# Kernel optimization log

Hardware: AMD Instinct MI355X
Metric: run time of the kernel (lower is better)

## Reference

```python
import jax, jax.numpy as jnp
import numpy as np

D = 64; H = 8; HD = 8; L = 3; FFN = 256
MAX_CHUNKS = 1024; MCL = 16


def rms_norm(x, w, eps=1e-6):
    return x * w * jax.lax.rsqrt(jnp.mean(x * x, axis=-1, keepdims=True) + eps)


def rope(x):
    # x: [B, S, H, HD]
    S, hd = x.shape[1], x.shape[-1]
    half = hd // 2
    freqs = 1.0 / (10000.0 ** (jnp.arange(half, dtype=x.dtype) * 2.0 / hd))
    ang = jnp.arange(S, dtype=x.dtype)[:, None] * freqs  # [S, half]
    cos = jnp.cos(ang)[None, :, None, :]
    sin = jnp.sin(ang)[None, :, None, :]
    x1, x2 = x[..., :half], x[..., half:]
    return jnp.concatenate([x1 * cos - x2 * sin, x1 * sin + x2 * cos], axis=-1)


def block(x, wq, wk, wv, wo, g1, g2, w1, w2):
    B, S, _ = x.shape
    h = rms_norm(x, g1)
    q = rope((h @ wq).reshape(B, S, H, HD))
    k = rope((h @ wk).reshape(B, S, H, HD))
    v = (h @ wv).reshape(B, S, H, HD)
    scores = jnp.einsum('bqhd,bkhd->bhqk', q, k) / jnp.sqrt(jnp.asarray(HD, x.dtype))
    causal = jnp.tril(jnp.ones((S, S), dtype=bool))
    scores = jnp.where(causal, scores, jnp.asarray(-1e30, x.dtype))
    attn = jax.nn.softmax(scores, axis=-1)
    o = jnp.einsum('bhqk,bkhd->bqhd', attn, v).reshape(B, S, D)
    x = x + o @ wo
    h2 = rms_norm(x, g2)
    return x + jax.nn.gelu(h2 @ w1, approximate=False) @ w2


def setup_inputs() -> dict:
    key = jax.random.key(0)
    ks = jax.random.split(key, 12)
    B, S = 4, 2048
    s = 1.0 / np.sqrt(D)
    return {
        'x': jax.random.normal(ks[0], (B, S, D), jnp.float32),
        'pad_token_vector': jax.random.normal(ks[1], (D,), jnp.float32),
        'x_ids': jax.random.randint(ks[2], (B, S), 0, 256),
        'pad_token_id': 257,
        'Wq': jax.random.normal(ks[3], (L, D, D), jnp.float32) * s,
        'Wk': jax.random.normal(ks[4], (L, D, D), jnp.float32) * s,
        'Wv': jax.random.normal(ks[5], (L, D, D), jnp.float32) * s,
        'Wo': jax.random.normal(ks[6], (L, D, D), jnp.float32) * s,
        'ln1': jnp.ones((L, D), jnp.float32),
        'ln2': jnp.ones((L, D), jnp.float32),
        'W1': jax.random.normal(ks[7], (L, D, FFN), jnp.float32) * s,
        'W2': jax.random.normal(ks[8], (L, FFN, D), jnp.float32) * (1.0 / np.sqrt(FFN)),
        'Whead': jax.random.normal(ks[9], (D, 2), jnp.float32) * s,
        'bhead': jnp.zeros((2,), jnp.float32),
    }


def reference(x, pad_token_vector, x_ids, pad_token_id, Wq, Wk, Wv, Wo, ln1, ln2, W1, W2, Whead, bhead):
    B, S, _ = x.shape
    h = x
    for l in range(L):
        h = block(h, Wq[l], Wk[l], Wv[l], Wo[l], ln1[l], ln2[l], W1[l], W2[l])
    logits = h @ Whead + bhead  # [B, S, 2]
    end_mask = logits[..., 0] > logits[..., 1]  # [B, S]
    t = jnp.arange(S)
    # fallback: if a row has no end, mark the last position as an end
    has_end = jnp.any(end_mask, axis=-1, keepdims=True)
    end_mask = jnp.where(has_end, end_mask, t[None, :] == S - 1)
    em = end_mask.astype(jnp.int32)
    num_ends = jnp.sum(em, axis=-1)                 # [B] = number of chunks
    chunk_id = jnp.cumsum(em, axis=-1) - em         # exclusive count of prior ends
    prev_end = jnp.concatenate([jnp.ones((B, 1), bool), end_mask[:, :-1]], axis=1)
    start_marker = jnp.where(prev_end, t[None, :], -1)
    start = jax.lax.associative_scan(jnp.maximum, start_marker, axis=-1)  # cummax -> chunk start per token
    pos = t[None, :] - start                        # position within chunk
    valid = (chunk_id < num_ends[:, None]) & (chunk_id < MAX_CHUNKS) & (pos < MCL)
    c_idx = jnp.where(valid, chunk_id, MAX_CHUNKS)  # invalid -> dummy chunk, sliced off
    p_idx = jnp.where(valid, pos, 0)
    b_idx = jnp.arange(B)[:, None]
    out = jnp.broadcast_to(pad_token_vector, (B, MAX_CHUNKS + 1, MCL, D))
    out = out.at[b_idx, c_idx, p_idx].set(h)[:, :MAX_CHUNKS]
    ids = jnp.full((B, MAX_CHUNKS + 1, MCL), pad_token_id, dtype=x_ids.dtype)
    ids = ids.at[b_idx, c_idx, p_idx].set(x_ids)[:, :MAX_CHUNKS]
    reg_term = jnp.mean(logits[..., 1])
    return out, ids, reg_term
```

## Files before the change

kernel.cpp:

```cpp
#include <hip/hip_runtime.h>
#include <math.h>

constexpr int D   = 64;
constexpr int H   = 8;
constexpr int HD  = 8;
constexpr int NL  = 3;
constexpr int FFNx= 256;
constexpr int Bb  = 4;
constexpr int Ss  = 2048;
constexpr int NT  = Bb * Ss;
constexpr int MAXC= 1024;
constexpr int MCL = 16;

constexpr int TPB  = 72;
constexpr int BPB  = 36;
constexpr int PBSZ = 2304;

constexpr size_t WX  = 0;
constexpr size_t WQ  = 524288;
constexpr size_t WKV = 2621440;
constexpr size_t WPB = 4194304;
constexpr size_t WL1 = 9764864;
constexpr size_t WEM = WL1 + NT;
constexpr size_t WINV= WEM + NT;
constexpr size_t WCT = WINV + Bb*MAXC*MCL;
constexpr size_t WST = WCT + Ss*4;

constexpr float LOG2E = 1.4426950408889634f;

typedef float v2f  __attribute__((ext_vector_type(2)));
typedef float f16v __attribute__((ext_vector_type(16)));
using ckv_t = const __attribute__((address_space(4))) f16v*;

__device__ __forceinline__ float rdlane(float v, int l) {
    return __builtin_bit_cast(float, __builtin_amdgcn_readlane(__builtin_bit_cast(int, v), l));
}

__global__ void k_init(const float* __restrict__ x, float* __restrict__ X,
                       float* __restrict__ ct, float* __restrict__ st) {
    int i = blockIdx.x * blockDim.x + threadIdx.x;
    constexpr int N4 = NT * D / 4;
    if (i < N4) ((float4*)X)[i] = ((const float4*)x)[i];
    if (i < Ss * 4) {
        int s = i >> 2, f = i & 3;
        const float fr[4] = {1.0f, 0.1f, 0.01f, 0.001f};
        float ang = (float)s * fr[f];
        ct[i] = cosf(ang);
        st[i] = sinf(ang);
    }
}

__global__ __launch_bounds__(256) void k_qkv(
    const float* __restrict__ X, const float* __restrict__ Wq,
    const float* __restrict__ Wk, const float* __restrict__ Wv,
    const float* __restrict__ g1, const float* __restrict__ ct,
    const float* __restrict__ st, float* __restrict__ Q,
    float* __restrict__ KV) {
    __shared__ float wq_s[D*D], wk_s[D*D], wv_s[D*D];
    __shared__ float g_s[D];
    int tid = threadIdx.x;
    for (int i = tid; i < D*D; i += 256) {
        wq_s[i] = Wq[i]; wk_s[i] = Wk[i]; wv_s[i] = Wv[i];
    }
    if (tid < D) g_s[tid] = g1[tid];
    __syncthreads();
    int w = tid >> 6, d = tid & 63;
    int t0 = blockIdx.x * 16;
    for (int it = 0; it < 4; ++it) {
        int t = t0 + it*4 + w;
        float xv = X[t*D + d];
        float ss = xv * xv;
        #pragma unroll
        for (int off = 32; off; off >>= 1) ss += __shfl_xor(ss, off);
        float r = 1.0f / sqrtf(ss * (1.0f/D) + 1e-6f);
        float h = xv * g_s[d] * r;
        float aq = 0.f, ak = 0.f, av = 0.f;
        #pragma unroll
        for (int j = 0; j < D; ++j) {
            float hj = rdlane(h, j);
            aq += hj * wq_s[j*D + d];
            ak += hj * wk_s[j*D + d];
            av += hj * wv_s[j*D + d];
        }
        int s  = t & (Ss - 1);
        int e  = d & 7;
        int fi = e & 3;
        float c  = ct[s*4 + fi];
        float sn = st[s*4 + fi];
        float pq = __shfl_xor(aq, 4);
        float pk = __shfl_xor(ak, 4);
        float rq, rk;
        if (e < 4) { rq = aq*c - pq*sn; rk = ak*c - pk*sn; }
        else       { rq = pq*sn + aq*c; rk = pk*sn + ak*c; }
        Q[t*D + d] = rq;
        int bq = t >> 11;
        int hh = d >> 3;
        float* kvp = KV + ((((size_t)(bq*H + hh))*Ss + s) << 4);
        kvp[e]     = rk;
        kvp[8 + e] = av;
    }
}

template<int DIAG>
__device__ __forceinline__ void attn_loop4(
    ckv_t kvs, int L, int rel0,
    const v2f* __restrict__ qp0, const v2f* __restrict__ qp1,
    v2f& l0, v2f& l1, v2f* __restrict__ o0, v2f* __restrict__ o1) {
    #pragma unroll 4
    for (int j = 0; j < 64; ++j) {
        f16v kv = kvs[j];
        v2f a1;
        a1  = qp1[0] * (v2f){kv[0], kv[0]};
        a1 += qp1[1] * (v2f){kv[1], kv[1]};
        a1 += qp1[2] * (v2f){kv[2], kv[2]};
        a1 += qp1[3] * (v2f){kv[3], kv[3]};
        a1 += qp1[4] * (v2f){kv[4], kv[4]};
        a1 += qp1[5] * (v2f){kv[5], kv[5]};
        a1 += qp1[6] * (v2f){kv[6], kv[6]};
        a1 += qp1[7] * (v2f){kv[7], kv[7]};
        if (DIAG == 2) {
            int rel = rel0 + j;
            if (rel > L)      a1.x = -1e30f;
            if (rel > L + 64) a1.y = -1e30f;
        }
        v2f p1;
        p1.x = __builtin_amdgcn_exp2f(a1.x);
        p1.y = __builtin_amdgcn_exp2f(a1.y);
        l1 += p1;
        o1[0] += p1 * (v2f){kv[8],  kv[8]};
        o1[1] += p1 * (v2f){kv[9],  kv[9]};
        o1[2] += p1 * (v2f){kv[10], kv[10]};
        o1[3] += p1 * (v2f){kv[11], kv[11]};
        o1[4] += p1 * (v2f){kv[12], kv[12]};
        o1[5] += p1 * (v2f){kv[13], kv[13]};
        o1[6] += p1 * (v2f){kv[14], kv[14]};
        o1[7] += p1 * (v2f){kv[15], kv[15]};
        if (DIAG != 2) {
            v2f a0;
            a0  = qp0[0] * (v2f){kv[0], kv[0]};
            a0 += qp0[1] * (v2f){kv[1], kv[1]};
            a0 += qp0[2] * (v2f){kv[2], kv[2]};
            a0 += qp0[3] * (v2f){kv[3], kv[3]};
            a0 += qp0[4] * (v2f){kv[4], kv[4]};
            a0 += qp0[5] * (v2f){kv[5], kv[5]};
            a0 += qp0[6] * (v2f){kv[6], kv[6]};
            a0 += qp0[7] * (v2f){kv[7], kv[7]};
            if (DIAG == 1) {
                int rel = rel0 + j;
                if (rel > L)      a0.x = -1e30f;
                if (rel > L + 64) a0.y = -1e30f;
            }
            v2f p0;
            p0.x = __builtin_amdgcn_exp2f(a0.x);
            p0.y = __builtin_amdgcn_exp2f(a0.y);
            l0 += p0;
            o0[0] += p0 * (v2f){kv[8],  kv[8]};
            o0[1] += p0 * (v2f){kv[9],  kv[9]};
            o0[2] += p0 * (v2f){kv[10], kv[10]};
            o0[3] += p0 * (v2f){kv[11], kv[11]};
            o0[4] += p0 * (v2f){kv[12], kv[12]};
            o0[5] += p0 * (v2f){kv[13], kv[13]};
            o0[6] += p0 * (v2f){kv[14], kv[14]};
            o0[7] += p0 * (v2f){kv[15], kv[15]};
        }
    }
}

__global__ __launch_bounds__(256) void k_attn2(
    const float* __restrict__ Qg, const float* __restrict__ KV,
    float* __restrict__ PB) {
    __shared__ float comb[2][PBSZ];
    int xcd  = blockIdx.x & 7;
    int slot = blockIdx.x >> 3;
    int bhg  = slot / BPB;
    int blk  = slot - bhg * BPB;
    int bh   = bhg * 8 + xcd;
    int wvu  = __builtin_amdgcn_readfirstlane(threadIdx.x >> 6);
    int pair = wvu >> 1;
    int half = wvu & 1;
    int widb = blk * 2 + pair;
    int L = threadIdx.x & 63;
    int rem = widb;
    int s = 0;
    while (rem >= 8 - (s >> 1)) { rem -= 8 - (s >> 1); ++s; }
    int t = (s >> 1) + rem;
    int b = bh >> 3, h = bh & 7;
    int qmin = t * 256;
    int k0 = s * 128 + half * 64;

    const float SC = 0.35355339059327373f * LOG2E;
    const float* qp = Qg + ((size_t)(b*Ss + qmin + L))*D + h*HD;
    float4 qa0 = *(const float4*)(qp);
    float4 qb0 = *(const float4*)(qp + 4);
    float4 qa1 = *(const float4*)(qp + 64*D);
    float4 qb1 = *(const float4*)(qp + 64*D + 4);
    float4 qa2 = *(const float4*)(qp + 128*D);
    float4 qb2 = *(const float4*)(qp + 128*D + 4);
    float4 qa3 = *(const float4*)(qp + 192*D);
    float4 qb3 = *(const float4*)(qp + 192*D + 4);
    v2f qp0[8], qp1[8];
    qp0[0] = (v2f){qa0.x*SC, qa1.x*SC};  qp1[0] = (v2f){qa2.x*SC, qa3.x*SC};
    qp0[1] = (v2f){qa0.y*SC, qa1.y*SC};  qp1[1] = (v2f){qa2.y*SC, qa3.y*SC};
    qp0[2] = (v2f){qa0.z*SC, qa1.z*SC};  qp1[2] = (v2f){qa2.z*SC, qa3.z*SC};
    qp0[3] = (v2f){qa0.w*SC, qa1.w*SC};  qp1[3] = (v2f){qa2.w*SC, qa3.w*SC};
    qp0[4] = (v2f){qb0.x*SC, qb1.x*SC};  qp1[4] = (v2f){qb2.x*SC, qb3.x*SC};
    qp0[5] = (v2f){qb0.y*SC, qb1.y*SC};  qp1[5] = (v2f){qb2.y*SC, qb3.y*SC};
    qp0[6] = (v2f){qb0.z*SC, qb1.z*SC};  qp1[6] = (v2f){qb2.z*SC, qb3.z*SC};
    qp0[7] = (v2f){qb0.w*SC, qb1.w*SC};  qp1[7] = (v2f){qb2.w*SC, qb3.w*SC};

    v2f l0 = (v2f){0.f, 0.f}, l1 = (v2f){0.f, 0.f};
    v2f o0[8], o1[8];
    #pragma unroll
    for (int e = 0; e < 8; ++e) { o0[e] = (v2f){0.f, 0.f}; o1[e] = (v2f){0.f, 0.f}; }

    ckv_t kvs = (ckv_t)(unsigned long long)(KV + (((size_t)bh*Ss + k0) << 4));
    if (s == 2*t)          attn_loop4<1>(kvs, L, half*64, qp0, qp1, l0, l1, o0, o1);
    else if (s == 2*t + 1) attn_loop4<2>(kvs, L, half*64, qp0, qp1, l0, l1, o0, o1);
    else                   attn_loop4<0>(kvs, L, half*64, qp0, qp1, l0, l1, o0, o1);

    if (half == 1) {
        comb[pair][L]       = l0.x;
        comb[pair][64 + L]  = l0.y;
        comb[pair][128 + L] = l1.x;
        comb[pair][192 + L] = l1.y;
        #pragma unroll
        for (int e = 0; e < 8; ++e) {
            comb[pair][256 + e*256 + L]       = o0[e].x;
            comb[pair][256 + e*256 + 64 + L]  = o0[e].y;
            comb[pair][256 + e*256 + 128 + L] = o1[e].x;
            comb[pair][256 + e*256 + 192 + L] = o1[e].y;
        }
    }
    __syncthreads();
    if (half == 0) {
        int pbidx = t*(t+1) + s;
        float* pb = PB + ((size_t)bh * TPB + pbidx) * PBSZ;
        pb[L]       = l0.x + comb[pair][L];
        pb[64 + L]  = l0.y + comb[pair][64 + L];
        pb[128 + L] = l1.x + comb[pair][128 + L];
        pb[192 + L] = l1.y + comb[pair][192 + L];
        #pragma unroll
        for (int e = 0; e < 8; ++e) {
            pb[256 + e*256 + L]       = o0[e].x + comb[pair][256 + e*256 + L];
            pb[256 + e*256 + 64 + L]  = o0[e].y + comb[pair][256 + e*256 + 64 + L];
            pb[256 + e*256 + 128 + L] = o1[e].x + comb[pair][256 + e*256 + 128 + L];
            pb[256 + e*256 + 192 + L] = o1[e].y + comb[pair][256 + e*256 + 192 + L];
        }
    }
}

__global__ __launch_bounds__(256) void k_combo(
    const float* __restrict__ PB, float* __restrict__ X,
    const float* __restrict__ Wo) {
    __shared__ float wo_s[D*D];
    __shared__ float oT[32][65];
    int tid = threadIdx.x;
    int seg = blockIdx.x & 7;
    int t   = (blockIdx.x >> 3) & 7;
    int b   = blockIdx.x >> 6;
    for (int i = tid; i < D*D; i += 256) wo_s[i] = Wo[i];

    int h  = tid >> 5;
    int ql = tid & 31;
    int qs = seg*32 + ql;
    int bh = b*8 + h;
    int nch = 2*(t+1);
    float Lx = 0.f;
    float O[8] = {0,0,0,0,0,0,0,0};
    for (int s3 = 0; s3 < nch; ++s3) {
        int idx = t*(t+1) + s3;
        const float* pb = PB + (size_t)(bh*TPB + idx) * PBSZ;
        Lx += pb[qs];
        #pragma unroll
        for (int e = 0; e < 8; ++e) O[e] += pb[256 + e*256 + qs];
    }
    float inv = 1.0f / Lx;
    #pragma unroll
    for (int e = 0; e < 8; ++e) oT[ql][h*8 + e] = O[e] * inv;
    __syncthreads();

    int d = tid & 63, wv = tid >> 6;
    #pragma unroll 2
    for (int k = 0; k < 8; ++k) {
        int tt = wv*8 + k;
        float a = 0.f;
        #pragma unroll
        for (int j = 0; j < D; ++j) a += oT[tt][j] * wo_s[j*D + d];
        X[((size_t)(b*Ss) + t*256 + seg*32 + tt)*D + d] += a;
    }
}

template<bool HEAD>
__global__ __launch_bounds__(256) void k_ffn(
    float* __restrict__ X, const float* __restrict__ g2,
    const float* __restrict__ W1, const float* __restrict__ W2,
    const float* __restrict__ Wh, const float* __restrict__ bhp,
    float* __restrict__ logit1, int* __restrict__ em) {
    __shared__ __align__(16) float h2t[64][20];
    __shared__ float part[16][16];
    __shared__ float g_s[D];
    __shared__ __align__(16) float ult[FFNx][20];
    __shared__ float red[4][16][D];
    int tid = threadIdx.x;
    if (tid < D) g_s[tid] = g2[tid];
    int t0 = blockIdx.x * 16;
    int tk = tid >> 4, li = tid & 15;
    float x0 = X[(t0+tk)*D + li];
    float x1 = X[(t0+tk)*D + li + 16];
    float x2 = X[(t0+tk)*D + li + 32];
    float x3 = X[(t0+tk)*D + li + 48];
    part[tk][li] = x0*x0 + x1*x1 + x2*x2 + x3*x3;
    __syncthreads();
    if (tid < 16) {
        float s = 0.f;
        #pragma unroll
        for (int i = 0; i < 16; ++i) s += part[tid][i];
        part[tid][0] = 1.0f / sqrtf(s * (1.0f/D) + 1e-6f);
    }
    __syncthreads();
    float r = part[tk][0];
    h2t[li][tk]      = x0 * g_s[li]      * r;
    h2t[li + 16][tk] = x1 * g_s[li + 16] * r;
    h2t[li + 32][tk] = x2 * g_s[li + 32] * r;
    h2t[li + 48][tk] = x3 * g_s[li + 48] * r;
    __syncthreads();
    {
        int f = tid;
        v2f acc2[8];
        #pragma unroll
        for (int i = 0; i < 8; ++i) acc2[i] = (v2f){0.f, 0.f};
        for (int j = 0; j < D; ++j) {
            float wv = W1[j*FFNx + f];
            v2f wv2 = (v2f){wv, wv};
            const float4* hp = (const float4*)&h2t[j][0];
            float4 a0 = hp[0], a1 = hp[1], a2 = hp[2], a3 = hp[3];
            const v2f* a0v = (const v2f*)&a0;
            const v2f* a1v = (const v2f*)&a1;
            const v2f* a2v = (const v2f*)&a2;
            const v2f* a3v = (const v2f*)&a3;
            acc2[0] += a0v[0]*wv2;  acc2[1] += a0v[1]*wv2;
            acc2[2] += a1v[0]*wv2;  acc2[3] += a1v[1]*wv2;
            acc2[4] += a2v[0]*wv2;  acc2[5] += a2v[1]*wv2;
            acc2[6] += a3v[0]*wv2;  acc2[7] += a3v[1]*wv2;
        }
        #pragma unroll
        for (int i = 0; i < 8; ++i) {
            float ua = acc2[i].x;
            float ub = acc2[i].y;
            ua = 0.5f * ua * (1.0f + erff(ua * 0.70710678118654752f));
            ub = 0.5f * ub * (1.0f + erff(ub * 0.70710678118654752f));
            ult[f][2*i]     = ua;
            ult[f][2*i + 1] = ub;
        }
    }
    __syncthreads();
    {
        int d = tid & 63, fp = tid >> 6;
        v2f acc2[8];
        #pragma unroll
        for (int i = 0; i < 8; ++i) acc2[i] = (v2f){0.f, 0.f};
        for (int fo = 0; fo < 64; ++fo) {
            int f = fp*64 + fo;
            float wv = W2[f*D + d];
            v2f wv2 = (v2f){wv, wv};
            const float4* up = (const float4*)&ult[f][0];
            float4 u0 = up[0], u1 = up[1], u2 = up[2], u3 = up[3];
            const v2f* u0v = (const v2f*)&u0;
            const v2f* u1v = (const v2f*)&u1;
            const v2f* u2v = (const v2f*)&u2;
            const v2f* u3v = (const v2f*)&u3;
            acc2[0] += u0v[0]*wv2;  acc2[1] += u0v[1]*wv2;
            acc2[2] += u1v[0]*wv2;  acc2[3] += u1v[1]*wv2;
            acc2[4] += u2v[0]*wv2;  acc2[5] += u2v[1]*wv2;
            acc2[6] += u3v[0]*wv2;  acc2[7] += u3v[1]*wv2;
        }
        #pragma unroll
        for (int i = 0; i < 8; ++i) {
            red[fp][2*i][d]     = acc2[i].x;
            red[fp][2*i + 1][d] = acc2[i].y;
        }
        __syncthreads();
        int tk2 = tid >> 6;
        #pragma unroll
        for (int k = 0; k < 4; ++k) {
            int tt = tk2 + k*4;
            float sum = red[0][tt][d] + red[1][tt][d] + red[2][tt][d] + red[3][tt][d];
            float xf = X[(t0 + tt)*D + d] + sum;
            X[(t0 + tt)*D + d] = xf;
            if (HEAD) {
                float p0 = xf * Wh[d*2];
                float p1 = xf * Wh[d*2 + 1];
                #pragma unroll
                for (int off = 32; off; off >>= 1) {
                    p0 += __shfl_xor(p0, off);
                    p1 += __shfl_xor(p1, off);
                }
                if (d == 0) {
                    float l0 = p0 + bhp[0], l1 = p1 + bhp[1];
                    em[t0 + tt] = (l0 > l1) ? 1 : 0;
                    logit1[t0 + tt] = l1;
                }
            }
        }
    }
}

__global__ void k_reg(const float* __restrict__ logit1, float* __restrict__ outreg) {
    __shared__ float red[256];
    int tid = threadIdx.x;
    float s = 0.f;
    for (int i = tid; i < NT; i += 256) s += logit1[i];
    red[tid] = s;
    __syncthreads();
    for (int off = 128; off; off >>= 1) {
        if (tid < off) red[tid] += red[tid + off];
        __syncthreads();
    }
    if (tid == 0) *outreg = red[0] * (1.0f / NT);
}

__global__ __launch_bounds__(256) void k_scan(const int* __restrict__ em,
                                              int* __restrict__ inv) {
    __shared__ int ssum[256], smax[256];
    __shared__ int sany, stot;
    int b = blockIdx.x, tid = threadIdx.x;
    int* invb = inv + b * (MAXC*MCL);
    for (int i = tid; i < MAXC*MCL; i += 256) invb[i] = -1;
    __syncthreads();
    const int* e = em + b*Ss;
    int base = tid * 8;
    int loc[8];
    int lsum = 0, lor = 0;
    #pragma unroll
    for (int i = 0; i < 8; ++i) { loc[i] = e[base + i]; lsum += loc[i]; lor |= loc[i]; }
    ssum[tid] = lor;
    __syncthreads();
    if (tid == 0) { int a = 0; for (int i = 0; i < 256; ++i) a |= ssum[i]; sany = a; }
    __syncthreads();
    int any = sany;
    __syncthreads();
    if (!any && tid == 255) { loc[7] = 1; lsum = 1; }
    int prev = (tid == 0) ? 1 : e[base - 1];
    if (!any && tid) prev = 0;
    int mk[8];
    int lmax = -1;
    #pragma unroll
    for (int i = 0; i < 8; ++i) {
        int pe = (i == 0) ? prev : loc[i - 1];
        if (i == 7 && !any && tid == 255) pe = e[base + 6];
        mk[i] = pe ? (base + i) : -1;
        lmax = max(lmax, mk[i]);
    }
    ssum[tid] = lsum; smax[tid] = lmax;
    __syncthreads();
    if (tid == 0) {
        int rs = 0, rm = -1;
        for (int i = 0; i < 256; ++i) {
            int ts = ssum[i], tm = smax[i];
            ssum[i] = rs; smax[i] = rm;
            rs += ts; rm = max(rm, tm);
        }
        stot = rs;
    }
    __syncthreads();
    int run = ssum[tid], rmax = smax[tid], tot = stot;
    #pragma unroll
    for (int i = 0; i < 8; ++i) {
        int s = base + i;
        rmax = max(rmax, mk[i]);
        int chunk = run;
        run += loc[i];
        int pos = s - rmax;
        bool valid = (chunk < tot) && (chunk < MAXC) && (pos < MCL);
        if (valid) invb[chunk * MCL + pos] = b*Ss + s;
    }
}

__global__ __launch_bounds__(256) void k_out(
    const float* __restrict__ X, const float* __restrict__ pad,
    const int* __restrict__ xids, const int* __restrict__ padid,
    const int* __restrict__ inv, float* __restrict__ out) {
    int i = blockIdx.x * blockDim.x + threadIdx.x;
    constexpr int NV4 = Bb * MAXC * MCL * D / 4;
    constexpr int NI4 = Bb * MAXC * MCL / 4;
    if (i < NV4) {
        int slot = i >> 4;
        int d4 = i & 15;
        int t = inv[slot];
        float4 v = (t >= 0) ? ((const float4*)X)[t*16 + d4]
                            : ((const float4*)pad)[d4];
        ((float4*)out)[i] = v;
    } else if (i < NV4 + NI4) {
        int j = i - NV4;
        float pv = (float)(*padid);
        int base = j * 4;
        int t0_ = inv[base], t1_ = inv[base+1], t2_ = inv[base+2], t3_ = inv[base+3];
        float4 v;
        v.x = (t0_ >= 0) ? (float)xids[t0_] : pv;
        v.y = (t1_ >= 0) ? (float)xids[t1_] : pv;
        v.z = (t2_ >= 0) ? (float)xids[t2_] : pv;
        v.w = (t3_ >= 0) ? (float)xids[t3_] : pv;
        ((float4*)out)[i] = v;
    }
}

extern "C" void kernel_launch(void* const* d_in, const int* in_sizes, int n_in,
                              void* d_out, int out_size, void* d_ws, size_t ws_size,
                              hipStream_t stream) {
    const float* x    = (const float*)d_in[0];
    const float* pad  = (const float*)d_in[1];
    const int*   xids = (const int*)  d_in[2];
    const int*   padid= (const int*)  d_in[3];
    const float* Wq   = (const float*)d_in[4];
    const float* Wk   = (const float*)d_in[5];
    const float* Wv   = (const float*)d_in[6];
    const float* Wo   = (const float*)d_in[7];
    const float* ln1  = (const float*)d_in[8];
    const float* ln2  = (const float*)d_in[9];
    const float* W1   = (const float*)d_in[10];
    const float* W2   = (const float*)d_in[11];
    const float* Wh   = (const float*)d_in[12];
    const float* bh   = (const float*)d_in[13];
    float* out = (float*)d_out;
    float* ws  = (float*)d_ws;

    float* X  = ws + WX;
    float* Qb = ws + WQ;
    float* KVb= ws + WKV;
    float* PBb= ws + WPB;
    float* L1b= ws + WL1;
    int*   EMb= (int*)(ws + WEM);
    int*   INVb=(int*)(ws + WINV);
    float* ct = ws + WCT;
    float* st = ws + WST;

    k_init<<<2048, 256, 0, stream>>>(x, X, ct, st);
    for (int l = 0; l < NL; ++l) {
        k_qkv <<<512, 256, 0, stream>>>(X, Wq + l*D*D, Wk + l*D*D, Wv + l*D*D,
                                        ln1 + l*D, ct, st, Qb, KVb);
        k_attn2<<<32*BPB, 256, 0, stream>>>(Qb, KVb, PBb);
        k_combo<<<256, 256, 0, stream>>>(PBb, X, Wo + l*D*D);
        if (l == NL - 1)
            k_ffn<true ><<<NT/16, 256, 0, stream>>>(X, ln2 + l*D, W1 + l*D*FFNx,
                                                    W2 + l*FFNx*D, Wh, bh, L1b, EMb);
        else
            k_ffn<false><<<NT/16, 256, 0, stream>>>(X, ln2 + l*D, W1 + l*D*FFNx,
                                                    W2 + l*FFNx*D, nullptr, nullptr,
                                                    nullptr, nullptr);
    }
    k_reg <<<1, 256, 0, stream>>>(L1b, out + (size_t)Bb*MAXC*MCL*D + Bb*MAXC*MCL);
    k_scan<<<Bb, 256, 0, stream>>>(EMb, INVb);
    k_out <<<(Bb*MAXC*MCL*D/4 + Bb*MAXC*MCL/4 + 255)/256, 256, 0, stream>>>(
        X, pad, xids, padid, INVb, out);
}
```

Before: 281.8 us.

## Fold RMSNorm gain into W1 and read FFN rows via scalar loads

A new prep kernel premultiplies W1 by the ln2 gain for every layer. This lets the FFN kernel skip building a normalized, transposed h2t tile in shared memory and apply the RMS scale after the dot product instead. Each thread now keeps its full W1 column in 64 registers and reads the token rows through constant-address-space (scalar) loads. The change removes one barrier and the LDS transpose, but it raises register pressure and turns the inner loop into per-token dot products.

```diff
diff --git a/kernel.cpp b/kernel.cpp
--- a/kernel.cpp
+++ b/kernel.cpp
@@ -25,6 +25,7 @@
 constexpr size_t WINV= WEM + NT;
 constexpr size_t WCT = WINV + Bb*MAXC*MCL;
 constexpr size_t WST = WCT + Ss*4;
+constexpr size_t WW1G= WST + Ss*4;
 
 constexpr float LOG2E = 1.4426950408889634f;
 
@@ -47,6 +48,16 @@
         float ang = (float)s * fr[f];
         ct[i] = cosf(ang);
         st[i] = sinf(ang);
+    }
+}
+
+__global__ void k_prep(const float* __restrict__ ln2, const float* __restrict__ W1,
+                       float* __restrict__ W1g) {
+    int i = blockIdx.x * blockDim.x + threadIdx.x;
+    if (i < NL * D * FFNx) {
+        int l = i / (D * FFNx);
+        int j = (i - l * D * FFNx) >> 8;
+        W1g[i] = ln2[l*D + j] * W1[i];
     }
 }
 
@@ -292,65 +303,49 @@
 
 template<bool HEAD>
 __global__ __launch_bounds__(256) void k_ffn(
-    float* __restrict__ X, const float* __restrict__ g2,
-    const float* __restrict__ W1, const float* __restrict__ W2,
+    float* __restrict__ X, const float* __restrict__ W1g,
+    const float* __restrict__ W2,
     const float* __restrict__ Wh, const float* __restrict__ bhp,
     float* __restrict__ logit1, int* __restrict__ em) {
-    __shared__ __align__(16) float h2t[64][20];
     __shared__ float part[16][16];
-    __shared__ float g_s[D];
+    __shared__ float rr[16];
     __shared__ __align__(16) float ult[FFNx][20];
     __shared__ float red[4][16][D];
     int tid = threadIdx.x;
-    if (tid < D) g_s[tid] = g2[tid];
     int t0 = blockIdx.x * 16;
     int tk = tid >> 4, li = tid & 15;
-    float x0 = X[(t0+tk)*D + li];
-    float x1 = X[(t0+tk)*D + li + 16];
-    float x2 = X[(t0+tk)*D + li + 32];
-    float x3 = X[(t0+tk)*D + li + 48];
-    part[tk][li] = x0*x0 + x1*x1 + x2*x2 + x3*x3;
+    {
+        float x0 = X[(t0+tk)*D + li];
+        float x1 = X[(t0+tk)*D + li + 16];
+        float x2 = X[(t0+tk)*D + li + 32];
+        float x3 = X[(t0+tk)*D + li + 48];
+        part[tk][li] = x0*x0 + x1*x1 + x2*x2 + x3*x3;
+    }
     __syncthreads();
     if (tid < 16) {
         float s = 0.f;
         #pragma unroll
         for (int i = 0; i < 16; ++i) s += part[tid][i];
-        part[tid][0] = 1.0f / sqrtf(s * (1.0f/D) + 1e-6f);
-    }
-    __syncthreads();
-    float r = part[tk][0];
-    h2t[li][tk]      = x0 * g_s[li]      * r;
-    h2t[li + 16][tk] = x1 * g_s[li + 16] * r;
-    h2t[li + 32][tk] = x2 * g_s[li + 32] * r;
-    h2t[li + 48][tk] = x3 * g_s[li + 48] * r;
+        rr[tid] = 1.0f / sqrtf(s * (1.0f/D) + 1e-6f);
+    }
     __syncthreads();
     {
         int f = tid;
-        v2f acc2[8];
-        #pragma unroll
-        for (int i = 0; i < 8; ++i) acc2[i] = (v2f){0.f, 0.f};
-        for (int j = 0; j < D; ++j) {
-            float wv = W1[j*FFNx + f];
-            v2f wv2 = (v2f){wv, wv};
-            const float4* hp = (const float4*)&h2t[j][0];
-            float4 a0 = hp[0], a1 = hp[1], a2 = hp[2], a3 = hp[3];
-            const v2f* a0v = (const v2f*)&a0;
-            const v2f* a1v = (const v2f*)&a1;
-            const v2f* a2v = (const v2f*)&a2;
-            const v2f* a3v = (const v2f*)&a3;
-            acc2[0] += a0v[0]*wv2;  acc2[1] += a0v[1]*wv2;
-            acc2[2] += a1v[0]*wv2;  acc2[3] += a1v[1]*wv2;
-            acc2[4] += a2v[0]*wv2;  acc2[5] += a2v[1]*wv2;
-            acc2[6] += a3v[0]*wv2;  acc2[7] += a3v[1]*wv2;
-        }
-        #pragma unroll
-        for (int i = 0; i < 8; ++i) {
-            float ua = acc2[i].x;
-            float ub = acc2[i].y;
-            ua = 0.5f * ua * (1.0f + erff(ua * 0.70710678118654752f));
-            ub = 0.5f * ub * (1.0f + erff(ub * 0.70710678118654752f));
-            ult[f][2*i]     = ua;
-            ult[f][2*i + 1] = ub;
+        float wcol[64];
+        #pragma unroll
+        for (int j = 0; j < 64; ++j) wcol[j] = W1g[j*FFNx + f];
+        for (int t = 0; t < 16; ++t) {
+            ckv_t xr = (ckv_t)(unsigned long long)(X + (size_t)(t0 + t)*D);
+            float acc = 0.f;
+            #pragma unroll
+            for (int q = 0; q < 4; ++q) {
+                f16v xs = xr[q];
+                #pragma unroll
+                for (int e = 0; e < 16; ++e) acc += xs[e] * wcol[q*16 + e];
+            }
+            float u = acc * rr[t];
+            u = 0.5f * u * (1.0f + erff(u * 0.70710678118654752f));
+            ult[f][t] = u;
         }
     }
     __syncthreads();
@@ -533,18 +528,20 @@
     int*   INVb=(int*)(ws + WINV);
     float* ct = ws + WCT;
     float* st = ws + WST;
+    float* W1Gb = ws + WW1G;
 
     k_init<<<2048, 256, 0, stream>>>(x, X, ct, st);
+    k_prep<<<(NL*D*FFNx + 255)/256, 256, 0, stream>>>(ln2, W1, W1Gb);
     for (int l = 0; l < NL; ++l) {
         k_qkv <<<512, 256, 0, stream>>>(X, Wq + l*D*D, Wk + l*D*D, Wv + l*D*D,
                                         ln1 + l*D, ct, st, Qb, KVb);
         k_attn2<<<32*BPB, 256, 0, stream>>>(Qb, KVb, PBb);
         k_combo<<<256, 256, 0, stream>>>(PBb, X, Wo + l*D*D);
         if (l == NL - 1)
-            k_ffn<true ><<<NT/16, 256, 0, stream>>>(X, ln2 + l*D, W1 + l*D*FFNx,
+            k_ffn<true ><<<NT/16, 256, 0, stream>>>(X, W1Gb + l*D*FFNx,
                                                     W2 + l*FFNx*D, Wh, bh, L1b, EMb);
         else
-            k_ffn<false><<<NT/16, 256, 0, stream>>>(X, ln2 + l*D, W1 + l*D*FFNx,
+            k_ffn<false><<<NT/16, 256, 0, stream>>>(X, W1Gb + l*D*FFNx,
                                                     W2 + l*FFNx*D, nullptr, nullptr,
                                                     nullptr, nullptr);
     }
```

After: 289.0 us. 2.6% more time.
